# Optimization experiments

Hardware: AMD Instinct MI355X
Metric: run time of the kernel (lower is better)

The kernel has to match this reference:

```python
import jax, jax.numpy as jnp
import numpy as np

B, S, D, H = 2, 2048, 1024, 16
HD = D // H  # head dim = 64

def setup_inputs() -> dict:
    key = jax.random.key(0)
    k1, k2, k3, k4, k5 = jax.random.split(key, 5)
    return {
        "x": jax.random.normal(k1, (B, S, D), dtype=jnp.float32),
        "w_qkv": jax.random.normal(k2, (D, 3 * D), dtype=jnp.float32) * (1.0 / np.sqrt(D)),
        "b_qkv": jax.random.normal(k3, (3 * D,), dtype=jnp.float32) * 0.02,
        "w_out": jax.random.normal(k4, (D, D), dtype=jnp.float32) * (1.0 / np.sqrt(D)),
        "b_out": jax.random.normal(k5, (D,), dtype=jnp.float32) * 0.02,
        "c": 0,
    }

def reference(x, w_qkv, b_qkv, w_out, b_out, c):
    # fused QKV projection: [B,S,3D]
    qkv = jnp.einsum('bsd,de->bse', x, w_qkv) + b_qkv
    q, k, v = jnp.split(qkv, 3, axis=-1)
    # [B,S,D] -> [B,H,S,HD]
    split_heads = lambda t: t.reshape(B, S, H, HD).transpose(0, 2, 1, 3)
    q, k, v = split_heads(q), split_heads(k), split_heads(v)
    scale = 1.0 / np.sqrt(HD).astype(np.float32)
    scores = jnp.einsum('bhqd,bhkd->bhqk', q, k) * scale  # [B,H,S,S]
    probs = jax.nn.softmax(scores, axis=-1)
    # c==1 noise path references an undefined `const` in the original (dead/broken);
    # dropout probs are 0 -> identity (eval mode).
    attn = jnp.einsum('bhqk,bhkd->bhqd', probs, v)  # [B,H,S,HD]
    attn = attn.transpose(0, 2, 1, 3).reshape(B, S, D)
    out = jnp.einsum('bsd,de->bse', attn, w_out) + b_out
    return out
```

## Files before the change

kernel.cpp:

```cpp
#include <hip/hip_runtime.h>


typedef __attribute__((ext_vector_type(8))) short bs8;
typedef __attribute__((ext_vector_type(4))) short bs4;
typedef __attribute__((ext_vector_type(4))) float f32x4;

__device__ __forceinline__ f32x4 MFMA16K16(bs4 a, bs4 b, f32x4 c) {
#if defined(__HIP_DEVICE_COMPILE__)
  return __builtin_amdgcn_mfma_f32_16x16x16bf16_1k(a, b, c, 0, 0, 0);
#else
  return c;
#endif
}

#define QSCALE 0.18033688011112042f
#define MBOUND 24.0f

__device__ __forceinline__ unsigned short f2bf(float f) {
  union { float f; unsigned int u; } v; v.f = f;
  return (unsigned short)((v.u + 0x8000u) >> 16);
}

__device__ __forceinline__ unsigned int pkbf2(float a, float b) {
  union { float f; unsigned int u; } va, vb; va.f = a; vb.f = b;
#if defined(__HIP_DEVICE_COMPILE__)
  return __builtin_amdgcn_perm(vb.u + 0x8000u, va.u + 0x8000u, 0x07060302u);
#else
  return 0u;
#endif
}

__device__ __forceinline__ void async16(const unsigned short* g, unsigned short* lds) {
  __builtin_amdgcn_global_load_lds(
      (const __attribute__((address_space(1))) unsigned int*)g,
      (__attribute__((address_space(3))) unsigned int*)lds, 16, 0, 0);
}

__device__ __forceinline__ void stage_rows64(unsigned short* lds, const unsigned short* src,
                                             int ldk, int w, int l) {
#pragma unroll
  for (int i = 0; i < 4; ++i) {
    int row = (w * 4 + i) * 8 + (l >> 3);
    int cg  = (l & 7) ^ (l >> 3);
    async16(src + (size_t)row * ldk + cg * 8, lds + (w * 4 + i) * 512);
  }
}

__device__ __forceinline__ void stage_rows64_8w(unsigned short* lds, const unsigned short* src,
                                                int ldk, int w, int l) {
#pragma unroll
  for (int i = 0; i < 2; ++i) {
    int row = (w * 2 + i) * 8 + (l >> 3);
    int cg  = (l & 7) ^ (l >> 3);
    async16(src + (size_t)row * ldk + cg * 8, lds + (w * 2 + i) * 512);
  }
}

__device__ __forceinline__ void stage_vt(unsigned short* lds, const unsigned short* vtb,
                                         int keyofs, int w, int l) {
#pragma unroll
  for (int i = 0; i < 4; ++i) {
    int row = (w * 4 + i) * 4 + (l >> 4);
    int cg = (l & 15) ^ (row & 15);
    async16(vtb + (size_t)row * 2048 + keyofs + cg * 8, lds + (w * 4 + i) * 512);
  }
}

__global__ __launch_bounds__(256) void cast_bf16_kernel(const float* __restrict__ src,
                                                        unsigned short* __restrict__ dst, int n) {
  int i = (blockIdx.x * 256 + threadIdx.x) * 8;
  if (i >= n) return;
  float4 a = *(const float4*)(src + i);
  float4 b = *(const float4*)(src + i + 4);
  union { bs8 v; unsigned short u[8]; } o;
  o.u[0] = f2bf(a.x); o.u[1] = f2bf(a.y); o.u[2] = f2bf(a.z); o.u[3] = f2bf(a.w);
  o.u[4] = f2bf(b.x); o.u[5] = f2bf(b.y); o.u[6] = f2bf(b.z); o.u[7] = f2bf(b.w);
  *(bs8*)(dst + i) = o.v;
}

__global__ __launch_bounds__(256) void transpose_cast_kernel(const float* __restrict__ src,
                                                             unsigned short* __restrict__ dst,
                                                             int R, int C) {
  __shared__ unsigned short tile[64][73];
  int c0 = blockIdx.x * 64, r0 = blockIdx.y * 64;
  int t = threadIdx.x;
  int rl = t >> 2, cb = (t & 3) * 16;
  const float* p = src + (size_t)(r0 + rl) * C + c0 + cb;
#pragma unroll
  for (int j = 0; j < 16; j += 4) {
    float4 f = *(const float4*)(p + j);
    tile[rl][cb + j + 0] = f2bf(f.x);
    tile[rl][cb + j + 1] = f2bf(f.y);
    tile[rl][cb + j + 2] = f2bf(f.z);
    tile[rl][cb + j + 3] = f2bf(f.w);
  }
  __syncthreads();
  int cl = t >> 2, rb = (t & 3) * 16;
  unsigned short* q = dst + (size_t)(c0 + cl) * R + r0 + rb;
#pragma unroll
  for (int j = 0; j < 16; ++j) q[j] = tile[rb + j][cl];
}

__global__ __launch_bounds__(256) void transpose_v_kernel(const unsigned short* __restrict__ v,
                                                          unsigned short* __restrict__ vt) {
  __shared__ unsigned short tile[64][73];
  int s0 = blockIdx.x * 64, bh = blockIdx.y;
  int t = threadIdx.x;
  int sl = t >> 2, hb = (t & 3) * 16;
  const unsigned short* p = v + ((size_t)bh * 2048 + s0 + sl) * 64 + hb;
#pragma unroll
  for (int j = 0; j < 16; ++j) tile[sl][hb + j] = p[j];
  __syncthreads();
  int hl = t >> 2, sb = (t & 3) * 16;
  unsigned short* q = vt + ((size_t)bh * 64 + hl) * 2048 + s0 + sb;
  int sw = (hl & 8) ? 4 : 0;
#pragma unroll
  for (int j = 0; j < 16; ++j) q[j ^ sw] = tile[sb + j][hl];
}

#define GEMM_CORE(A_, Bt_)                                                        \
  __shared__ unsigned short As[128 * 64];                                         \
  __shared__ unsigned short Bs[128 * 64];                                         \
  int t = threadIdx.x, w = t >> 6, l = t & 63;                                    \
  int wm = w >> 1, wn = w & 1;                                                    \
  int bm = blockIdx.y, bn = blockIdx.x;                                           \
  const unsigned short* Abase = (A_) + (size_t)bm * 128 * 1024;                   \
  const unsigned short* Bbase = (Bt_) + (size_t)bn * 128 * 1024;                  \
  f32x4 zero4 = {0.f, 0.f, 0.f, 0.f};                                             \
  f32x4 acc[4][4];                                                                \
  _Pragma("unroll") for (int i = 0; i < 4; ++i)                                   \
  _Pragma("unroll") for (int j = 0; j < 4; ++j) acc[i][j] = zero4;                \
  for (int kt = 0; kt < 16; ++kt) {                                               \
    stage_rows64(As, Abase + kt * 64, 1024, w, l);                                \
    stage_rows64(Bs, Bbase + kt * 64, 1024, w, l);                                \
    __syncthreads();                                                              \
    _Pragma("unroll") for (int ks = 0; ks < 2; ++ks) {                            \
      bs8 af[4], bf[4];                                                           \
      _Pragma("unroll") for (int mt = 0; mt < 4; ++mt) {                          \
        int row = wm * 64 + mt * 16 + (l & 15);                                   \
        int c = ks * 4 + (l >> 4);                                                \
        af[mt] = *(const bs8*)&As[row * 64 + ((c ^ (row & 7)) * 8)];              \
      }                                                                           \
      _Pragma("unroll") for (int nt = 0; nt < 4; ++nt) {                          \
        int row = wn * 64 + nt * 16 + (l & 15);                                   \
        int c = ks * 4 + (l >> 4);                                                \
        bf[nt] = *(const bs8*)&Bs[row * 64 + ((c ^ (row & 7)) * 8)];              \
      }                                                                           \
      _Pragma("unroll") for (int mt = 0; mt < 4; ++mt)                            \
      _Pragma("unroll") for (int nt = 0; nt < 4; ++nt)                            \
        acc[mt][nt] = __builtin_amdgcn_mfma_f32_16x16x32_bf16(af[mt], bf[nt],     \
                                                              acc[mt][nt], 0, 0, 0); \
    }                                                                             \
    __syncthreads();                                                              \
  }

__global__ __launch_bounds__(256) void gemm_qkv_kernel(const unsigned short* __restrict__ A,
                                                       const unsigned short* __restrict__ Bt,
                                                       const float* __restrict__ bias,
                                                       unsigned short* __restrict__ qo,
                                                       unsigned short* __restrict__ ko,
                                                       unsigned short* __restrict__ vo) {
  GEMM_CORE(A, Bt)
#pragma unroll
  for (int nt = 0; nt < 4; ++nt) {
    int ng = bn * 128 + wn * 64 + nt * 16 + (l & 15);
    float bb = bias[ng];
    int sect = ng >> 10;
    int f = ng & 1023, h = f >> 6, hd = f & 63;
    unsigned short* dst = (sect == 0) ? qo : (sect == 1) ? ko : vo;
    float sc = (sect == 0) ? QSCALE : 1.0f;
#pragma unroll
    for (int mt = 0; mt < 4; ++mt)
#pragma unroll
      for (int r = 0; r < 4; ++r) {
        int mg = bm * 128 + wm * 64 + mt * 16 + (l >> 4) * 4 + r;
        int b = mg >> 11, s = mg & 2047;
        float val = (acc[mt][nt][r] + bb) * sc;
        dst[((size_t)(b * 16 + h) * 2048 + s) * 64 + hd] = f2bf(val);
      }
  }
}

__global__ __launch_bounds__(512) void gemm_out_kernel(const unsigned short* __restrict__ A,
                                                       const unsigned short* __restrict__ Bt,
                                                       const float* __restrict__ bias,
                                                       float* __restrict__ out) {
  __shared__ unsigned short As[128 * 64];
  __shared__ unsigned short Bs[128 * 64];
  int t = threadIdx.x, w = t >> 6, l = t & 63;
  int wm = w >> 1, wn = w & 1;
  int bm = blockIdx.y, bn = blockIdx.x;
  const unsigned short* Abase = A + (size_t)bm * 128 * 1024;
  const unsigned short* Bbase = Bt + (size_t)bn * 128 * 1024;
  f32x4 zero4 = {0.f, 0.f, 0.f, 0.f};
  f32x4 acc[2][4];
#pragma unroll
  for (int i = 0; i < 2; ++i)
#pragma unroll
    for (int j = 0; j < 4; ++j) acc[i][j] = zero4;
  for (int kt = 0; kt < 16; ++kt) {
    stage_rows64_8w(As, Abase + kt * 64, 1024, w, l);
    stage_rows64_8w(Bs, Bbase + kt * 64, 1024, w, l);
    __syncthreads();
#pragma unroll
    for (int ks = 0; ks < 2; ++ks) {
      bs8 af[2], bf[4];
#pragma unroll
      for (int mt = 0; mt < 2; ++mt) {
        int row = wm * 32 + mt * 16 + (l & 15);
        int c = ks * 4 + (l >> 4);
        af[mt] = *(const bs8*)&As[row * 64 + ((c ^ (row & 7)) * 8)];
      }
#pragma unroll
      for (int nt = 0; nt < 4; ++nt) {
        int row = wn * 64 + nt * 16 + (l & 15);
        int c = ks * 4 + (l >> 4);
        bf[nt] = *(const bs8*)&Bs[row * 64 + ((c ^ (row & 7)) * 8)];
      }
#pragma unroll
      for (int mt = 0; mt < 2; ++mt)
#pragma unroll
        for (int nt = 0; nt < 4; ++nt)
          acc[mt][nt] = __builtin_amdgcn_mfma_f32_16x16x32_bf16(af[mt], bf[nt],
                                                                acc[mt][nt], 0, 0, 0);
    }
    __syncthreads();
  }
#pragma unroll
  for (int nt = 0; nt < 4; ++nt) {
    int ng = bn * 128 + wn * 64 + nt * 16 + (l & 15);
    float bb = bias[ng];
#pragma unroll
    for (int mt = 0; mt < 2; ++mt)
#pragma unroll
      for (int r = 0; r < 4; ++r) {
        int mg = bm * 128 + wm * 32 + mt * 16 + (l >> 4) * 4 + r;
        out[(size_t)mg * 1024 + ng] = acc[mt][nt][r] + bb;
      }
  }
}

__global__ __launch_bounds__(256, 2) void attn_kernel(const unsigned short* __restrict__ Q,
                                                      const unsigned short* __restrict__ K,
                                                      const unsigned short* __restrict__ Vt,
                                                      unsigned short* __restrict__ Aout) {
  __shared__ unsigned short Ks[2][128 * 64];
  __shared__ unsigned short Vts[2][64 * 128];
  int t = threadIdx.x, w = t >> 6, l = t & 63;
  int m16 = l & 15, q = l >> 4;
  int qt = blockIdx.x, bh = blockIdx.y;
  const unsigned short* qbase = Q + (size_t)bh * 2048 * 64 + (size_t)qt * 128 * 64;
  const unsigned short* kbase = K + (size_t)bh * 2048 * 64;
  const unsigned short* vtbase = Vt + (size_t)bh * 64 * 2048;

  bs8 qf[2][2];
#pragma unroll
  for (int mt = 0; mt < 2; ++mt)
#pragma unroll
    for (int ks = 0; ks < 2; ++ks)
      qf[mt][ks] = *(const bs8*)(qbase + (size_t)(w * 32 + mt * 16 + m16) * 64 + ks * 32 + q * 8);

  stage_rows64(&Ks[0][0], kbase, 64, w, l);
  stage_vt(&Vts[0][0], vtbase, 0, w, l);
  __syncthreads();

  f32x4 minit = {-MBOUND, -MBOUND, -MBOUND, -MBOUND};
  f32x4 zero4 = {0.f, 0.f, 0.f, 0.f};
  f32x4 o[2][4];
  float lst[2] = {0.f, 0.f};
#pragma unroll
  for (int mt = 0; mt < 2; ++mt)
#pragma unroll
    for (int nh = 0; nh < 4; ++nh) o[mt][nh] = zero4;

  int vsw = (m16 >> 3) & 1;

  for (int kt = 0; kt < 16; ++kt) {
    int buf = kt & 1;
    if (kt < 15) {
      stage_rows64(&Ks[buf ^ 1][0], kbase + (size_t)(kt + 1) * 128 * 64, 64, w, l);
      stage_vt(&Vts[buf ^ 1][0], vtbase, (kt + 1) * 128, w, l);
    }
    const unsigned short* Kb = &Ks[buf][0];
    const unsigned short* Vb = &Vts[buf][0];

    f32x4 sAcc[2][8];
#pragma unroll
    for (int mt = 0; mt < 2; ++mt)
#pragma unroll
      for (int nt = 0; nt < 8; ++nt) sAcc[mt][nt] = minit;
#pragma unroll
    for (int ks = 0; ks < 2; ++ks) {
      bs8 kf[8];
#pragma unroll
      for (int nt = 0; nt < 8; ++nt) {
        int row = nt * 16 + m16;
        int c = ks * 4 + q;
        kf[nt] = *(const bs8*)&Kb[row * 64 + ((c ^ (row & 7)) * 8)];
      }
#pragma unroll
      for (int nt = 0; nt < 8; ++nt)
#pragma unroll
        for (int mt = 0; mt < 2; ++mt)
          sAcc[mt][nt] = __builtin_amdgcn_mfma_f32_16x16x32_bf16(kf[nt], qf[mt][ks],
                                                                 sAcc[mt][nt], 0, 0, 0);
    }

#pragma unroll
    for (int mt = 0; mt < 2; ++mt) {
      float rs = 0.f;
#pragma unroll
      for (int nt = 0; nt < 8; ++nt)
#pragma unroll
        for (int r = 0; r < 4; ++r) {
          float p = __builtin_amdgcn_exp2f(sAcc[mt][nt][r]);
          sAcc[mt][nt][r] = p;
          rs += p;
        }
      lst[mt] += rs;
    }

#pragma unroll
    for (int nt = 0; nt < 8; ++nt) {
      bs4 vf[4];
#pragma unroll
      for (int nh = 0; nh < 4; ++nh) {
        int vrow = nh * 16 + m16;
        int chunk = nt * 2 + (q >> 1);
        int within = ((q & 1) ^ vsw) * 4;
        vf[nh] = *(const bs4*)&Vb[vrow * 128 + ((chunk ^ (vrow & 15)) * 8) + within];
      }
#pragma unroll
      for (int mt = 0; mt < 2; ++mt) {
        union { bs4 v; unsigned int u[2]; } pf;
        pf.u[0] = pkbf2(sAcc[mt][nt][0], sAcc[mt][nt][1]);
        pf.u[1] = pkbf2(sAcc[mt][nt][2], sAcc[mt][nt][3]);
#pragma unroll
        for (int nh = 0; nh < 4; ++nh)
          o[mt][nh] = MFMA16K16(vf[nh], pf.v, o[mt][nh]);
      }
    }
    __syncthreads();
  }

  int b = bh >> 4, h = bh & 15;
#pragma unroll
  for (int mt = 0; mt < 2; ++mt) {
    float l0 = lst[mt];
    l0 += __shfl_xor(l0, 16);
    l0 += __shfl_xor(l0, 32);
    float inv = 1.0f / l0;
    int s = qt * 128 + w * 32 + mt * 16 + m16;
#pragma unroll
    for (int nh = 0; nh < 4; ++nh)
#pragma unroll
      for (int r = 0; r < 4; ++r) {
        int hd = nh * 16 + q * 4 + r;
        Aout[((size_t)(b * 2048 + s)) * 1024 + h * 64 + hd] = f2bf(o[mt][nh][r] * inv);
      }
  }
}

extern "C" void kernel_launch(void* const* d_in, const int* in_sizes, int n_in,
                              void* d_out, int out_size, void* d_ws, size_t ws_size,
                              hipStream_t stream) {
  const float* x     = (const float*)d_in[0];
  const float* w_qkv = (const float*)d_in[1];
  const float* b_qkv = (const float*)d_in[2];
  const float* w_out = (const float*)d_in[3];
  const float* b_out = (const float*)d_in[4];
  float* out = (float*)d_out;

  char* ws = (char*)d_ws;
  unsigned short* xb    = (unsigned short*)(ws);
  unsigned short* wt1   = (unsigned short*)(ws + (8u << 20));
  unsigned short* wt2   = (unsigned short*)(ws + (14u << 20));
  unsigned short* qb    = (unsigned short*)(ws + (16u << 20));
  unsigned short* kb    = (unsigned short*)(ws + (24u << 20));
  unsigned short* vb    = (unsigned short*)(ws + (32u << 20));
  unsigned short* vtb   = (unsigned short*)(ws + (40u << 20));
  unsigned short* attnb = (unsigned short*)(ws + (48u << 20));

  cast_bf16_kernel<<<2048, 256, 0, stream>>>(x, xb, 4194304);
  transpose_cast_kernel<<<dim3(48, 16), 256, 0, stream>>>(w_qkv, wt1, 1024, 3072);
  transpose_cast_kernel<<<dim3(16, 16), 256, 0, stream>>>(w_out, wt2, 1024, 1024);
  gemm_qkv_kernel<<<dim3(24, 32), 256, 0, stream>>>(xb, wt1, b_qkv, qb, kb, vb);
  transpose_v_kernel<<<dim3(32, 32), 256, 0, stream>>>(vb, vtb);
  attn_kernel<<<dim3(16, 32), 256, 0, stream>>>(qb, kb, vtb, attnb);
  gemm_out_kernel<<<dim3(8, 32), 512, 0, stream>>>(attnb, wt2, b_out, out);
}
```

Measured before the change: 206.4 us.

## Restructure attention to 8 waves of 16 query rows with 64-key tiles

Result: slower. 215.1 us (+4.2%).

```diff
diff --git a/kernel.cpp b/kernel.cpp
--- a/kernel.cpp
+++ b/kernel.cpp
@@ -56,14 +56,11 @@
   }
 }
 
-__device__ __forceinline__ void stage_vt(unsigned short* lds, const unsigned short* vtb,
-                                         int keyofs, int w, int l) {
-#pragma unroll
-  for (int i = 0; i < 4; ++i) {
-    int row = (w * 4 + i) * 4 + (l >> 4);
-    int cg = (l & 15) ^ (row & 15);
-    async16(vtb + (size_t)row * 2048 + keyofs + cg * 8, lds + (w * 4 + i) * 512);
-  }
+__device__ __forceinline__ void stage64x64(unsigned short* lds, const unsigned short* src,
+                                           int ldk, int w, int l) {
+  int row = w * 8 + (l >> 3);
+  int cg  = (l & 7) ^ (l >> 3);
+  async16(src + (size_t)row * ldk + cg * 8, lds + w * 512);
 }
 
 __global__ __launch_bounds__(256) void cast_bf16_kernel(const float* __restrict__ src,
@@ -240,12 +237,12 @@
   }
 }
 
-__global__ __launch_bounds__(256, 2) void attn_kernel(const unsigned short* __restrict__ Q,
+__global__ __launch_bounds__(512, 4) void attn_kernel(const unsigned short* __restrict__ Q,
                                                       const unsigned short* __restrict__ K,
                                                       const unsigned short* __restrict__ Vt,
                                                       unsigned short* __restrict__ Aout) {
-  __shared__ unsigned short Ks[2][128 * 64];
-  __shared__ unsigned short Vts[2][64 * 128];
+  __shared__ unsigned short Ks[2][64 * 64];
+  __shared__ unsigned short Vts[2][64 * 64];
   int t = threadIdx.x, w = t >> 6, l = t & 63;
   int m16 = l & 15, q = l >> 4;
   int qt = blockIdx.x, bh = blockIdx.y;
@@ -253,112 +250,95 @@
   const unsigned short* kbase = K + (size_t)bh * 2048 * 64;
   const unsigned short* vtbase = Vt + (size_t)bh * 64 * 2048;
 
-  bs8 qf[2][2];
-#pragma unroll
-  for (int mt = 0; mt < 2; ++mt)
-#pragma unroll
-    for (int ks = 0; ks < 2; ++ks)
-      qf[mt][ks] = *(const bs8*)(qbase + (size_t)(w * 32 + mt * 16 + m16) * 64 + ks * 32 + q * 8);
-
-  stage_rows64(&Ks[0][0], kbase, 64, w, l);
-  stage_vt(&Vts[0][0], vtbase, 0, w, l);
+  bs8 qf[2];
+#pragma unroll
+  for (int ks = 0; ks < 2; ++ks)
+    qf[ks] = *(const bs8*)(qbase + (size_t)(w * 16 + m16) * 64 + ks * 32 + q * 8);
+
+  stage64x64(&Ks[0][0], kbase, 64, w, l);
+  stage64x64(&Vts[0][0], vtbase, 2048, w, l);
   __syncthreads();
 
   f32x4 minit = {-MBOUND, -MBOUND, -MBOUND, -MBOUND};
   f32x4 zero4 = {0.f, 0.f, 0.f, 0.f};
-  f32x4 o[2][4];
-  float lst[2] = {0.f, 0.f};
-#pragma unroll
-  for (int mt = 0; mt < 2; ++mt)
-#pragma unroll
-    for (int nh = 0; nh < 4; ++nh) o[mt][nh] = zero4;
+  f32x4 o[4];
+  float lsum = 0.f;
+#pragma unroll
+  for (int nh = 0; nh < 4; ++nh) o[nh] = zero4;
 
   int vsw = (m16 >> 3) & 1;
 
-  for (int kt = 0; kt < 16; ++kt) {
+  for (int kt = 0; kt < 32; ++kt) {
     int buf = kt & 1;
-    if (kt < 15) {
-      stage_rows64(&Ks[buf ^ 1][0], kbase + (size_t)(kt + 1) * 128 * 64, 64, w, l);
-      stage_vt(&Vts[buf ^ 1][0], vtbase, (kt + 1) * 128, w, l);
+    if (kt < 31) {
+      stage64x64(&Ks[buf ^ 1][0], kbase + (size_t)(kt + 1) * 64 * 64, 64, w, l);
+      stage64x64(&Vts[buf ^ 1][0], vtbase + (size_t)(kt + 1) * 64, 2048, w, l);
     }
     const unsigned short* Kb = &Ks[buf][0];
     const unsigned short* Vb = &Vts[buf][0];
 
-    f32x4 sAcc[2][8];
-#pragma unroll
-    for (int mt = 0; mt < 2; ++mt)
-#pragma unroll
-      for (int nt = 0; nt < 8; ++nt) sAcc[mt][nt] = minit;
+    f32x4 sAcc[4];
+#pragma unroll
+    for (int nt = 0; nt < 4; ++nt) sAcc[nt] = minit;
 #pragma unroll
     for (int ks = 0; ks < 2; ++ks) {
-      bs8 kf[8];
-#pragma unroll
-      for (int nt = 0; nt < 8; ++nt) {
+      bs8 kf[4];
+#pragma unroll
+      for (int nt = 0; nt < 4; ++nt) {
         int row = nt * 16 + m16;
         int c = ks * 4 + q;
         kf[nt] = *(const bs8*)&Kb[row * 64 + ((c ^ (row & 7)) * 8)];
       }
 #pragma unroll
-      for (int nt = 0; nt < 8; ++nt)
-#pragma unroll
-        for (int mt = 0; mt < 2; ++mt)
-          sAcc[mt][nt] = __builtin_amdgcn_mfma_f32_16x16x32_bf16(kf[nt], qf[mt][ks],
-                                                                 sAcc[mt][nt], 0, 0, 0);
-    }
-
-#pragma unroll
-    for (int mt = 0; mt < 2; ++mt) {
-      float rs = 0.f;
-#pragma unroll
-      for (int nt = 0; nt < 8; ++nt)
-#pragma unroll
-        for (int r = 0; r < 4; ++r) {
-          float p = __builtin_amdgcn_exp2f(sAcc[mt][nt][r]);
-          sAcc[mt][nt][r] = p;
-          rs += p;
-        }
-      lst[mt] += rs;
-    }
-
-#pragma unroll
-    for (int nt = 0; nt < 8; ++nt) {
+      for (int nt = 0; nt < 4; ++nt)
+        sAcc[nt] = __builtin_amdgcn_mfma_f32_16x16x32_bf16(kf[nt], qf[ks],
+                                                           sAcc[nt], 0, 0, 0);
+    }
+
+    float rs = 0.f;
+#pragma unroll
+    for (int nt = 0; nt < 4; ++nt)
+#pragma unroll
+      for (int r = 0; r < 4; ++r) {
+        float p = __builtin_amdgcn_exp2f(sAcc[nt][r]);
+        sAcc[nt][r] = p;
+        rs += p;
+      }
+    lsum += rs;
+
+#pragma unroll
+    for (int nt = 0; nt < 4; ++nt) {
       bs4 vf[4];
 #pragma unroll
       for (int nh = 0; nh < 4; ++nh) {
         int vrow = nh * 16 + m16;
         int chunk = nt * 2 + (q >> 1);
         int within = ((q & 1) ^ vsw) * 4;
-        vf[nh] = *(const bs4*)&Vb[vrow * 128 + ((chunk ^ (vrow & 15)) * 8) + within];
-      }
-#pragma unroll
-      for (int mt = 0; mt < 2; ++mt) {
-        union { bs4 v; unsigned int u[2]; } pf;
-        pf.u[0] = pkbf2(sAcc[mt][nt][0], sAcc[mt][nt][1]);
-        pf.u[1] = pkbf2(sAcc[mt][nt][2], sAcc[mt][nt][3]);
-#pragma unroll
-        for (int nh = 0; nh < 4; ++nh)
-          o[mt][nh] = MFMA16K16(vf[nh], pf.v, o[mt][nh]);
-      }
+        vf[nh] = *(const bs4*)&Vb[vrow * 64 + ((chunk ^ (vrow & 7)) * 8) + within];
+      }
+      union { bs4 v; unsigned int u[2]; } pf;
+      pf.u[0] = pkbf2(sAcc[nt][0], sAcc[nt][1]);
+      pf.u[1] = pkbf2(sAcc[nt][2], sAcc[nt][3]);
+#pragma unroll
+      for (int nh = 0; nh < 4; ++nh)
+        o[nh] = MFMA16K16(vf[nh], pf.v, o[nh]);
     }
     __syncthreads();
   }
 
   int b = bh >> 4, h = bh & 15;
-#pragma unroll
-  for (int mt = 0; mt < 2; ++mt) {
-    float l0 = lst[mt];
-    l0 += __shfl_xor(l0, 16);
-    l0 += __shfl_xor(l0, 32);
-    float inv = 1.0f / l0;
-    int s = qt * 128 + w * 32 + mt * 16 + m16;
-#pragma unroll
-    for (int nh = 0; nh < 4; ++nh)
-#pragma unroll
-      for (int r = 0; r < 4; ++r) {
-        int hd = nh * 16 + q * 4 + r;
-        Aout[((size_t)(b * 2048 + s)) * 1024 + h * 64 + hd] = f2bf(o[mt][nh][r] * inv);
-      }
-  }
+  float l0 = lsum;
+  l0 += __shfl_xor(l0, 16);
+  l0 += __shfl_xor(l0, 32);
+  float inv = 1.0f / l0;
+  int s = qt * 128 + w * 16 + m16;
+#pragma unroll
+  for (int nh = 0; nh < 4; ++nh)
+#pragma unroll
+    for (int r = 0; r < 4; ++r) {
+      int hd = nh * 16 + q * 4 + r;
+      Aout[((size_t)(b * 2048 + s)) * 1024 + h * 64 + hd] = f2bf(o[nh][r] * inv);
+    }
 }
 
 extern "C" void kernel_launch(void* const* d_in, const int* in_sizes, int n_in,
@@ -386,6 +366,6 @@
   transpose_cast_kernel<<<dim3(16, 16), 256, 0, stream>>>(w_out, wt2, 1024, 1024);
   gemm_qkv_kernel<<<dim3(24, 32), 256, 0, stream>>>(xb, wt1, b_qkv, qb, kb, vb);
   transpose_v_kernel<<<dim3(32, 32), 256, 0, stream>>>(vb, vtb);
-  attn_kernel<<<dim3(16, 32), 256, 0, stream>>>(qb, kb, vtb, attnb);
+  attn_kernel<<<dim3(16, 32), 512, 0, stream>>>(qb, kb, vtb, attnb);
   gemm_out_kernel<<<dim3(8, 32), 512, 0, stream>>>(attnb, wt2, b_out, out);
 }
```

## Fuse V transpose into QKV GEMM epilogue and split attention keys across 8 waves

Applied to the files above, without the earlier changes.

Measured after the change: 196.3 us. -4.9%, faster.

```diff
diff --git a/kernel.cpp b/kernel.cpp
--- a/kernel.cpp
+++ b/kernel.cpp
@@ -56,13 +56,13 @@
   }
 }
 
-__device__ __forceinline__ void stage_vt(unsigned short* lds, const unsigned short* vtb,
-                                         int keyofs, int w, int l) {
-#pragma unroll
-  for (int i = 0; i < 4; ++i) {
-    int row = (w * 4 + i) * 4 + (l >> 4);
+__device__ __forceinline__ void stage_vt_8w(unsigned short* lds, const unsigned short* vtb,
+                                            int keyofs, int w, int l) {
+#pragma unroll
+  for (int i = 0; i < 2; ++i) {
+    int row = (w * 2 + i) * 4 + (l >> 4);
     int cg = (l & 15) ^ (row & 15);
-    async16(vtb + (size_t)row * 2048 + keyofs + cg * 8, lds + (w * 4 + i) * 512);
+    async16(vtb + (size_t)row * 2048 + keyofs + cg * 8, lds + (w * 2 + i) * 512);
   }
 }
 
@@ -99,23 +99,6 @@
   unsigned short* q = dst + (size_t)(c0 + cl) * R + r0 + rb;
 #pragma unroll
   for (int j = 0; j < 16; ++j) q[j] = tile[rb + j][cl];
-}
-
-__global__ __launch_bounds__(256) void transpose_v_kernel(const unsigned short* __restrict__ v,
-                                                          unsigned short* __restrict__ vt) {
-  __shared__ unsigned short tile[64][73];
-  int s0 = blockIdx.x * 64, bh = blockIdx.y;
-  int t = threadIdx.x;
-  int sl = t >> 2, hb = (t & 3) * 16;
-  const unsigned short* p = v + ((size_t)bh * 2048 + s0 + sl) * 64 + hb;
-#pragma unroll
-  for (int j = 0; j < 16; ++j) tile[sl][hb + j] = p[j];
-  __syncthreads();
-  int hl = t >> 2, sb = (t & 3) * 16;
-  unsigned short* q = vt + ((size_t)bh * 64 + hl) * 2048 + s0 + sb;
-  int sw = (hl & 8) ? 4 : 0;
-#pragma unroll
-  for (int j = 0; j < 16; ++j) q[j ^ sw] = tile[sb + j][hl];
 }
 
 #define GEMM_CORE(A_, Bt_)                                                        \
@@ -159,7 +142,7 @@
                                                        const float* __restrict__ bias,
                                                        unsigned short* __restrict__ qo,
                                                        unsigned short* __restrict__ ko,
-                                                       unsigned short* __restrict__ vo) {
+                                                       unsigned short* __restrict__ vto) {
   GEMM_CORE(A, Bt)
 #pragma unroll
   for (int nt = 0; nt < 4; ++nt) {
@@ -167,17 +150,29 @@
     float bb = bias[ng];
     int sect = ng >> 10;
     int f = ng & 1023, h = f >> 6, hd = f & 63;
-    unsigned short* dst = (sect == 0) ? qo : (sect == 1) ? ko : vo;
-    float sc = (sect == 0) ? QSCALE : 1.0f;
-#pragma unroll
-    for (int mt = 0; mt < 4; ++mt)
-#pragma unroll
-      for (int r = 0; r < 4; ++r) {
-        int mg = bm * 128 + wm * 64 + mt * 16 + (l >> 4) * 4 + r;
-        int b = mg >> 11, s = mg & 2047;
-        float val = (acc[mt][nt][r] + bb) * sc;
-        dst[((size_t)(b * 16 + h) * 2048 + s) * 64 + hd] = f2bf(val);
-      }
+    if (sect == 2) {
+      int sw4 = (hd & 8) ? 4 : 0;
+#pragma unroll
+      for (int mt = 0; mt < 4; ++mt) {
+        int mg0 = bm * 128 + wm * 64 + mt * 16 + (l >> 4) * 4;
+        int b = mg0 >> 11, s0 = (mg0 & 2047) ^ sw4;
+        union { bs4 v; unsigned short u[4]; } pv;
+#pragma unroll
+        for (int r = 0; r < 4; ++r) pv.u[r] = f2bf(acc[mt][nt][r] + bb);
+        *(bs4*)&vto[((size_t)(b * 16 + h) * 64 + hd) * 2048 + s0] = pv.v;
+      }
+    } else {
+      unsigned short* dst = (sect == 0) ? qo : ko;
+      float sc = (sect == 0) ? QSCALE : 1.0f;
+#pragma unroll
+      for (int mt = 0; mt < 4; ++mt)
+#pragma unroll
+        for (int r = 0; r < 4; ++r) {
+          int mg = bm * 128 + wm * 64 + mt * 16 + (l >> 4) * 4 + r;
+          int b = mg >> 11, s = mg & 2047;
+          dst[((size_t)(b * 16 + h) * 2048 + s) * 64 + hd] = f2bf((acc[mt][nt][r] + bb) * sc);
+        }
+    }
   }
 }
 
@@ -240,7 +235,7 @@
   }
 }
 
-__global__ __launch_bounds__(256, 2) void attn_kernel(const unsigned short* __restrict__ Q,
+__global__ __launch_bounds__(512, 4) void attn_kernel(const unsigned short* __restrict__ Q,
                                                       const unsigned short* __restrict__ K,
                                                       const unsigned short* __restrict__ Vt,
                                                       unsigned short* __restrict__ Aout) {
@@ -248,6 +243,7 @@
   __shared__ unsigned short Vts[2][64 * 128];
   int t = threadIdx.x, w = t >> 6, l = t & 63;
   int m16 = l & 15, q = l >> 4;
+  int wq = w & 3, kh = w >> 2;
   int qt = blockIdx.x, bh = blockIdx.y;
   const unsigned short* qbase = Q + (size_t)bh * 2048 * 64 + (size_t)qt * 128 * 64;
   const unsigned short* kbase = K + (size_t)bh * 2048 * 64;
@@ -258,16 +254,16 @@
   for (int mt = 0; mt < 2; ++mt)
 #pragma unroll
     for (int ks = 0; ks < 2; ++ks)
-      qf[mt][ks] = *(const bs8*)(qbase + (size_t)(w * 32 + mt * 16 + m16) * 64 + ks * 32 + q * 8);
-
-  stage_rows64(&Ks[0][0], kbase, 64, w, l);
-  stage_vt(&Vts[0][0], vtbase, 0, w, l);
+      qf[mt][ks] = *(const bs8*)(qbase + (size_t)(wq * 32 + mt * 16 + m16) * 64 + ks * 32 + q * 8);
+
+  stage_rows64_8w(&Ks[0][0], kbase, 64, w, l);
+  stage_vt_8w(&Vts[0][0], vtbase, 0, w, l);
   __syncthreads();
 
   f32x4 minit = {-MBOUND, -MBOUND, -MBOUND, -MBOUND};
   f32x4 zero4 = {0.f, 0.f, 0.f, 0.f};
   f32x4 o[2][4];
-  float lst[2] = {0.f, 0.f};
+  float lsum[2] = {0.f, 0.f};
 #pragma unroll
   for (int mt = 0; mt < 2; ++mt)
 #pragma unroll
@@ -278,28 +274,28 @@
   for (int kt = 0; kt < 16; ++kt) {
     int buf = kt & 1;
     if (kt < 15) {
-      stage_rows64(&Ks[buf ^ 1][0], kbase + (size_t)(kt + 1) * 128 * 64, 64, w, l);
-      stage_vt(&Vts[buf ^ 1][0], vtbase, (kt + 1) * 128, w, l);
+      stage_rows64_8w(&Ks[buf ^ 1][0], kbase + (size_t)(kt + 1) * 128 * 64, 64, w, l);
+      stage_vt_8w(&Vts[buf ^ 1][0], vtbase, (kt + 1) * 128, w, l);
     }
     const unsigned short* Kb = &Ks[buf][0];
     const unsigned short* Vb = &Vts[buf][0];
 
-    f32x4 sAcc[2][8];
+    f32x4 sAcc[2][4];
 #pragma unroll
     for (int mt = 0; mt < 2; ++mt)
 #pragma unroll
-      for (int nt = 0; nt < 8; ++nt) sAcc[mt][nt] = minit;
+      for (int nt = 0; nt < 4; ++nt) sAcc[mt][nt] = minit;
 #pragma unroll
     for (int ks = 0; ks < 2; ++ks) {
-      bs8 kf[8];
-#pragma unroll
-      for (int nt = 0; nt < 8; ++nt) {
-        int row = nt * 16 + m16;
+      bs8 kf[4];
+#pragma unroll
+      for (int nt = 0; nt < 4; ++nt) {
+        int row = kh * 64 + nt * 16 + m16;
         int c = ks * 4 + q;
         kf[nt] = *(const bs8*)&Kb[row * 64 + ((c ^ (row & 7)) * 8)];
       }
 #pragma unroll
-      for (int nt = 0; nt < 8; ++nt)
+      for (int nt = 0; nt < 4; ++nt)
 #pragma unroll
         for (int mt = 0; mt < 2; ++mt)
           sAcc[mt][nt] = __builtin_amdgcn_mfma_f32_16x16x32_bf16(kf[nt], qf[mt][ks],
@@ -310,23 +306,23 @@
     for (int mt = 0; mt < 2; ++mt) {
       float rs = 0.f;
 #pragma unroll
-      for (int nt = 0; nt < 8; ++nt)
+      for (int nt = 0; nt < 4; ++nt)
 #pragma unroll
         for (int r = 0; r < 4; ++r) {
           float p = __builtin_amdgcn_exp2f(sAcc[mt][nt][r]);
           sAcc[mt][nt][r] = p;
           rs += p;
         }
-      lst[mt] += rs;
-    }
-
-#pragma unroll
-    for (int nt = 0; nt < 8; ++nt) {
+      lsum[mt] += rs;
+    }
+
+#pragma unroll
+    for (int nt = 0; nt < 4; ++nt) {
       bs4 vf[4];
 #pragma unroll
       for (int nh = 0; nh < 4; ++nh) {
         int vrow = nh * 16 + m16;
-        int chunk = nt * 2 + (q >> 1);
+        int chunk = kh * 8 + nt * 2 + (q >> 1);
         int within = ((q & 1) ^ vsw) * 4;
         vf[nh] = *(const bs4*)&Vb[vrow * 128 + ((chunk ^ (vrow & 15)) * 8) + within];
       }
@@ -343,21 +339,46 @@
     __syncthreads();
   }
 
-  int b = bh >> 4, h = bh & 15;
-#pragma unroll
-  for (int mt = 0; mt < 2; ++mt) {
-    float l0 = lst[mt];
-    l0 += __shfl_xor(l0, 16);
-    l0 += __shfl_xor(l0, 32);
-    float inv = 1.0f / l0;
-    int s = qt * 128 + w * 32 + mt * 16 + m16;
-#pragma unroll
-    for (int nh = 0; nh < 4; ++nh)
-#pragma unroll
-      for (int r = 0; r < 4; ++r) {
-        int hd = nh * 16 + q * 4 + r;
-        Aout[((size_t)(b * 2048 + s)) * 1024 + h * 64 + hd] = f2bf(o[mt][nh][r] * inv);
-      }
+  float* ored = (float*)&Ks[0][0];
+  float* lred = (float*)&Vts[0][0];
+  if (w >= 4) {
+#pragma unroll
+    for (int mt = 0; mt < 2; ++mt)
+#pragma unroll
+      for (int nh = 0; nh < 4; ++nh)
+        *(f32x4*)&ored[((mt * 4 + nh) * 256 + wq * 64 + l) * 4] = o[mt][nh];
+    lred[0 * 256 + wq * 64 + l] = lsum[0];
+    lred[1 * 256 + wq * 64 + l] = lsum[1];
+  }
+  __syncthreads();
+  if (w < 4) {
+#pragma unroll
+    for (int mt = 0; mt < 2; ++mt)
+#pragma unroll
+      for (int nh = 0; nh < 4; ++nh) {
+        f32x4 part = *(const f32x4*)&ored[((mt * 4 + nh) * 256 + wq * 64 + l) * 4];
+#pragma unroll
+        for (int r = 0; r < 4; ++r) o[mt][nh][r] += part[r];
+      }
+    lsum[0] += lred[0 * 256 + wq * 64 + l];
+    lsum[1] += lred[1 * 256 + wq * 64 + l];
+
+    int b = bh >> 4, h = bh & 15;
+#pragma unroll
+    for (int mt = 0; mt < 2; ++mt) {
+      float l0 = lsum[mt];
+      l0 += __shfl_xor(l0, 16);
+      l0 += __shfl_xor(l0, 32);
+      float inv = 1.0f / l0;
+      int s = qt * 128 + wq * 32 + mt * 16 + m16;
+#pragma unroll
+      for (int nh = 0; nh < 4; ++nh)
+#pragma unroll
+        for (int r = 0; r < 4; ++r) {
+          int hd = nh * 16 + q * 4 + r;
+          Aout[((size_t)(b * 2048 + s)) * 1024 + h * 64 + hd] = f2bf(o[mt][nh][r] * inv);
+        }
+    }
   }
 }
 
@@ -377,15 +398,13 @@
   unsigned short* wt2   = (unsigned short*)(ws + (14u << 20));
   unsigned short* qb    = (unsigned short*)(ws + (16u << 20));
   unsigned short* kb    = (unsigned short*)(ws + (24u << 20));
-  unsigned short* vb    = (unsigned short*)(ws + (32u << 20));
-  unsigned short* vtb   = (unsigned short*)(ws + (40u << 20));
-  unsigned short* attnb = (unsigned short*)(ws + (48u << 20));
+  unsigned short* vtb   = (unsigned short*)(ws + (32u << 20));
+  unsigned short* attnb = (unsigned short*)(ws + (40u << 20));
 
   cast_bf16_kernel<<<2048, 256, 0, stream>>>(x, xb, 4194304);
   transpose_cast_kernel<<<dim3(48, 16), 256, 0, stream>>>(w_qkv, wt1, 1024, 3072);
   transpose_cast_kernel<<<dim3(16, 16), 256, 0, stream>>>(w_out, wt2, 1024, 1024);
-  gemm_qkv_kernel<<<dim3(24, 32), 256, 0, stream>>>(xb, wt1, b_qkv, qb, kb, vb);
-  transpose_v_kernel<<<dim3(32, 32), 256, 0, stream>>>(vb, vtb);
-  attn_kernel<<<dim3(16, 32), 256, 0, stream>>>(qb, kb, vtb, attnb);
+  gemm_qkv_kernel<<<dim3(24, 32), 256, 0, stream>>>(xb, wt1, b_qkv, qb, kb, vtb);
+  attn_kernel<<<dim3(16, 32), 512, 0, stream>>>(qb, kb, vtb, attnb);
   gemm_out_kernel<<<dim3(8, 32), 512, 0, stream>>>(attnb, wt2, b_out, out);
 }
```
